# Optimization experiments

Hardware: AMD Instinct MI355X
Metric: run time of the kernel (lower is better)

The kernel has to match this reference:

```python
import jax, jax.numpy as jnp
import numpy as np

D_MODEL = 1024
NHEAD = 16
HEAD_DIM = D_MODEL // NHEAD


def setup_inputs() -> dict:
    key = jax.random.key(0)
    ks = jax.random.split(key, 6)
    scale = 0.02
    x = jax.random.normal(ks[0], (8, 1024, D_MODEL), dtype=jnp.float32)
    # nn.Linear weights are [out, in]; per-head q/k/v stacked over heads
    W_split = jax.random.normal(ks[1], (D_MODEL, D_MODEL), dtype=jnp.float32) * scale
    W_out = jax.random.normal(ks[2], (D_MODEL, D_MODEL), dtype=jnp.float32) * scale
    Wq = jax.random.normal(ks[3], (NHEAD, HEAD_DIM, HEAD_DIM), dtype=jnp.float32) * scale
    Wk = jax.random.normal(ks[4], (NHEAD, HEAD_DIM, HEAD_DIM), dtype=jnp.float32) * scale
    Wv = jax.random.normal(ks[5], (NHEAD, HEAD_DIM, HEAD_DIM), dtype=jnp.float32) * scale
    return {"x": x, "W_split": W_split, "W_out": W_out, "Wq": Wq, "Wk": Wk, "Wv": Wv}


def reference(x, W_split, W_out, Wq, Wk, Wv):
    b, s, _ = x.shape
    # x_proj: [b, s, h, hd]
    xp = (x @ W_split.T).reshape(b, s, NHEAD, HEAD_DIM)
    # per-head Linear (weight [out,in]): y = x @ W.T
    q = jnp.einsum('bshd,hod->bsho', xp, Wq)
    k = jnp.einsum('bshd,hod->bsho', xp, Wk)
    v = jnp.einsum('bshd,hod->bsho', xp, Wv)
    # scores scaled by sqrt(head_dim) (Attention.d_model == head_dim)
    scores = jnp.einsum('bsho,btho->bhst', q, k) / jnp.sqrt(jnp.float32(HEAD_DIM))
    attn = jax.nn.softmax(scores, axis=-1)  # [b, h, s, s]
    out = jnp.einsum('bhst,btho->bsho', attn, v)  # [b, s, h, hd]
    concat = out.reshape(b, s, D_MODEL)
    return concat @ W_out.T
```

## Files before the change

kernel.cpp:

```cpp
#include <hip/hip_runtime.h>
#include <math.h>

#define NHEAD 16
#define HD 64
#define DMODEL 1024
#define SEQ 1024
#define BATCH 8
#define ROWS (BATCH * SEQ)

typedef __attribute__((ext_vector_type(8))) short bf16x8;
typedef __attribute__((ext_vector_type(8))) short short8v;
typedef __attribute__((ext_vector_type(4))) float f32x4;
typedef __attribute__((ext_vector_type(16))) float f32x16;
typedef __attribute__((ext_vector_type(4))) short short4v;
typedef __attribute__((ext_vector_type(4))) unsigned int uint32x4;

__device__ __forceinline__ unsigned short f2bf(float f) {
    unsigned u = __builtin_bit_cast(unsigned, f);
    u += 0x7FFF + ((u >> 16) & 1);
    return (unsigned short)(u >> 16);
}

__device__ __forceinline__ float fexp2(float x) {
#if __has_builtin(__builtin_amdgcn_exp2f)
    return __builtin_amdgcn_exp2f(x);
#else
    return __expf(x * 0.6931471805599453f);
#endif
}

__device__ __forceinline__ void gload16(const void* g, void* l) {
    __builtin_amdgcn_global_load_lds(
        (const __attribute__((address_space(1))) unsigned int*)g,
        (__attribute__((address_space(3))) unsigned int*)l, 16, 0, 0);
}

__global__ __launch_bounds__(256) void cvt_bf16(const float* __restrict__ src,
                                                unsigned short* __restrict__ dst,
                                                int n, float scale) {
    int i = (blockIdx.x * 256 + threadIdx.x) * 8;
    if (i >= n) return;
    float4 a = *(const float4*)(src + i);
    float4 b = *(const float4*)(src + i + 4);
    short8v o;
    o[0] = (short)f2bf(a.x * scale); o[1] = (short)f2bf(a.y * scale);
    o[2] = (short)f2bf(a.z * scale); o[3] = (short)f2bf(a.w * scale);
    o[4] = (short)f2bf(b.x * scale); o[5] = (short)f2bf(b.y * scale);
    o[6] = (short)f2bf(b.z * scale); o[7] = (short)f2bf(b.w * scale);
    *(short8v*)(dst + i) = o;
}

__global__ __launch_bounds__(256) void gemm1_qkv(const unsigned short* __restrict__ A,
                                                 const unsigned short* __restrict__ B,
                                                 const unsigned short* __restrict__ wqb,
                                                 const unsigned short* __restrict__ wkb,
                                                 const unsigned short* __restrict__ wvb,
                                                 unsigned short* __restrict__ qb,
                                                 unsigned short* __restrict__ kbuf,
                                                 unsigned short* __restrict__ vT) {
    __shared__ char lds[65536];
    const int tid  = threadIdx.x;
    const int w    = tid >> 6;
    const int lane = tid & 63;
    const int lr   = lane & 15, lg = lane >> 4;
    const int wr   = w >> 1,  wc = w & 1;
    const int m0   = blockIdx.x * 128;
    const int n0   = blockIdx.y * 128;
    const int K    = DMODEL;

    f32x4 acc[4][4] = {};

    const int srow   = lane >> 3;
    const int swbyte = ((lane & 7) ^ srow) << 4;

#define G1_STAGE(buf, k0)                                                          \
    {                                                                              \
        _Pragma("unroll")                                                          \
        for (int c = 0; c < 4; ++c) {                                              \
            int chunk = w * 4 + c;                                                 \
            int row   = chunk * 8 + srow;                                          \
            gload16((const char*)A + ((size_t)(m0 + row) * K + (k0)) * 2 + swbyte, \
                    lds + (buf) * 16384 + chunk * 1024);                           \
            gload16((const char*)B + ((size_t)(n0 + row) * K + (k0)) * 2 + swbyte, \
                    lds + 32768 + (buf) * 16384 + chunk * 1024);                   \
        }                                                                          \
    }

    G1_STAGE(0, 0);
    __syncthreads();

    int cur = 0;
    for (int t = 0; t < K / 64; ++t) {
        if (t + 1 < K / 64) G1_STAGE(cur ^ 1, (t + 1) * 64);

#pragma unroll
        for (int k2 = 0; k2 < 2; ++k2) {
            bf16x8 af[4], bg[4];
#pragma unroll
            for (int f = 0; f < 4; ++f) {
                int row = wr * 64 + f * 16 + lr;
                af[f] = *(const bf16x8*)(lds + cur * 16384 + row * 128 +
                                         ((k2 * 64 + lg * 16) ^ ((row & 7) << 4)));
            }
#pragma unroll
            for (int g = 0; g < 4; ++g) {
                int row = wc * 64 + g * 16 + lr;
                bg[g] = *(const bf16x8*)(lds + 32768 + cur * 16384 + row * 128 +
                                         ((k2 * 64 + lg * 16) ^ ((row & 7) << 4)));
            }
#pragma unroll
            for (int f = 0; f < 4; ++f)
#pragma unroll
                for (int g = 0; g < 4; ++g)
                    acc[f][g] = __builtin_amdgcn_mfma_f32_16x16x32_bf16(af[f], bg[g],
                                                                        acc[f][g], 0, 0, 0);
        }
        __syncthreads();
        cur ^= 1;
    }
#undef G1_STAGE

#pragma unroll
    for (int f = 0; f < 4; ++f)
#pragma unroll
        for (int g = 0; g < 4; ++g)
#pragma unroll
            for (int r = 0; r < 4; ++r) {
                int mrow = wr * 64 + f * 16 + lg * 4 + r;
                int ncol = wc * 64 + g * 16 + lr;
                *(unsigned short*)(lds + mrow * 256 + ((ncol * 2) ^ ((mrow & 7) << 4))) =
                    f2bf(acc[f][g][r]);
            }

    const int b  = m0 >> 10;
    const int sl = m0 & 1023;

#pragma unroll
    for (int hh = 0; hh < 2; ++hh) {
        const int h = blockIdx.y * 2 + hh;
#pragma unroll
        for (int i = 0; i < 6; ++i) {
            int c   = w * 6 + i;
            int p   = c >> 3, rc = c & 7;
            int row = rc * 8 + srow;
            const unsigned short* ws = (p == 0) ? wqb : (p == 1) ? wkb : wvb;
            gload16((const char*)ws + ((size_t)(h * 64 + row) * 64) * 2 + swbyte,
                    lds + 32768 + p * 8192 + rc * 1024);
        }
        __syncthreads();

        f32x4 a2[3][2][4] = {};
#pragma unroll
        for (int k2 = 0; k2 < 2; ++k2) {
            bf16x8 af[2];
#pragma unroll
            for (int f = 0; f < 2; ++f) {
                int row = w * 32 + f * 16 + lr;
                af[f] = *(const bf16x8*)(lds + row * 256 +
                                         ((hh * 128 + k2 * 64 + lg * 16) ^ ((row & 7) << 4)));
            }
#pragma unroll
            for (int p = 0; p < 3; ++p)
#pragma unroll
                for (int g = 0; g < 4; ++g) {
                    int o = g * 16 + lr;
                    bf16x8 bg = *(const bf16x8*)(lds + 32768 + p * 8192 + o * 128 +
                                                 ((k2 * 64 + lg * 16) ^ ((o & 7) << 4)));
#pragma unroll
                    for (int f = 0; f < 2; ++f)
                        a2[p][f][g] = __builtin_amdgcn_mfma_f32_16x16x32_bf16(af[f], bg,
                                                                              a2[p][f][g], 0, 0, 0);
                }
        }

#pragma unroll
        for (int f = 0; f < 2; ++f)
#pragma unroll
            for (int g = 0; g < 4; ++g) {
#pragma unroll
                for (int r = 0; r < 4; ++r) {
                    size_t idx = (size_t)(m0 + w * 32 + f * 16 + lg * 4 + r) * DMODEL +
                                 h * 64 + g * 16 + lr;
                    qb[idx]   = f2bf(a2[0][f][g][r]);
                    kbuf[idx] = f2bf(a2[1][f][g][r]);
                }
                short4v pv;
#pragma unroll
                for (int r = 0; r < 4; ++r) pv[r] = (short)f2bf(a2[2][f][g][r]);
                size_t o = (size_t)(b * 16 + h) * 64 + g * 16 + lr;
                *(short4v*)(vT + o * SEQ + sl + w * 32 + f * 16 + lg * 4) = pv;
            }
        __syncthreads();
    }
}

__global__ __launch_bounds__(256) void gemm_bf16(const unsigned short* __restrict__ A,
                                                 const unsigned short* __restrict__ B,
                                                 float* __restrict__ Cf,
                                                 int M, int N, int K) {
    __shared__ char sA[2][16384];
    __shared__ char sB[2][16384];
    const int tid  = threadIdx.x;
    const int w    = tid >> 6;
    const int lane = tid & 63;
    const int lr   = lane & 15, lg = lane >> 4;
    const int wr   = w >> 1,  wc = w & 1;
    const int m0   = blockIdx.x * 128;
    const int n0   = blockIdx.y * 128;

    f32x4 acc[4][4] = {};

    const int srow   = lane >> 3;
    const int swbyte = ((lane & 7) ^ srow) << 4;
    const int nt     = K / 64;

#define GEMM_STAGE(buf, k0)                                                        \
    {                                                                              \
        _Pragma("unroll")                                                          \
        for (int c = 0; c < 4; ++c) {                                              \
            int chunk = w * 4 + c;                                                 \
            int row   = chunk * 8 + srow;                                          \
            gload16((const char*)A + ((size_t)(m0 + row) * K + (k0)) * 2 + swbyte, \
                    sA[buf] + chunk * 1024);                                       \
            gload16((const char*)B + ((size_t)(n0 + row) * K + (k0)) * 2 + swbyte, \
                    sB[buf] + chunk * 1024);                                       \
        }                                                                          \
    }

    GEMM_STAGE(0, 0);
    __syncthreads();

    int cur = 0;
    for (int t = 0; t < nt; ++t) {
        if (t + 1 < nt) GEMM_STAGE(cur ^ 1, (t + 1) * 64);

#pragma unroll
        for (int k2 = 0; k2 < 2; ++k2) {
            bf16x8 af[4], bg[4];
#pragma unroll
            for (int f = 0; f < 4; ++f) {
                int row = wr * 64 + f * 16 + lr;
                af[f] = *(const bf16x8*)(sA[cur] + row * 128 +
                                         ((k2 * 64 + lg * 16) ^ ((row & 7) << 4)));
            }
#pragma unroll
            for (int g = 0; g < 4; ++g) {
                int row = wc * 64 + g * 16 + lr;
                bg[g] = *(const bf16x8*)(sB[cur] + row * 128 +
                                         ((k2 * 64 + lg * 16) ^ ((row & 7) << 4)));
            }
#pragma unroll
            for (int f = 0; f < 4; ++f)
#pragma unroll
                for (int g = 0; g < 4; ++g)
                    acc[f][g] = __builtin_amdgcn_mfma_f32_16x16x32_bf16(af[f], bg[g],
                                                                        acc[f][g], 0, 0, 0);
        }
        __syncthreads();
        cur ^= 1;
    }
#undef GEMM_STAGE

#pragma unroll
    for (int f = 0; f < 4; ++f)
#pragma unroll
        for (int g = 0; g < 4; ++g)
#pragma unroll
            for (int r = 0; r < 4; ++r)
                Cf[(size_t)(m0 + wr * 64 + f * 16 + lg * 4 + r) * N +
                   n0 + wc * 64 + g * 16 + lr] = acc[f][g][r];
}

__global__ __launch_bounds__(512) void attn_mfma(const unsigned short* __restrict__ qb,
                                                 const unsigned short* __restrict__ kb,
                                                 const unsigned short* __restrict__ vT,
                                                 unsigned short* __restrict__ ob) {
    __shared__ unsigned short sK[4][4096];
    __shared__ unsigned short sV[4][4096];

    const int tid  = threadIdx.x;
    const int w    = tid >> 6;
    const int lane = tid & 63;
    const int ql   = lane & 31;
    const int hl   = lane >> 5;
    const int bh   = blockIdx.x;
    const int b    = bh >> 4, h = bh & 15;
    const int s0   = blockIdx.y * 256;
    const int NT   = SEQ / 64;

    const unsigned short* qrow = qb + ((size_t)(b * SEQ + s0 + w * 32 + ql) * DMODEL + h * 64);
    bf16x8 qf[4];
#pragma unroll
    for (int s = 0; s < 4; ++s)
        qf[s] = *(const bf16x8*)(qrow + 16 * s + 8 * hl);

    f32x16 acc0 = {}, acc1 = {};
    float m_ = -1e30f, l_ = 0.f;

    const int srow = lane >> 3;
    const int ssw  = ((lane & 7) << 4) ^ (srow << 4);
    const int swz  = (ql & 7) << 4;

#define ATTN_STAGE(buf, kt)                                                          \
    {                                                                                \
        int row = w * 8 + srow;                                                      \
        gload16((const char*)kb +                                                    \
                    (((size_t)(b * SEQ + (kt) * 64 + row) * DMODEL + h * 64) * 2) + ssw, \
                (char*)sK[buf] + w * 1024);                                          \
        gload16((const char*)vT +                                                    \
                    (((size_t)(bh * 64 + row) * SEQ + (kt) * 64) * 2) + ssw,         \
                (char*)sV[buf] + w * 1024);                                          \
    }

    ATTN_STAGE(0, 0);
    ATTN_STAGE(1, 1);
    asm volatile("s_waitcnt vmcnt(2)" ::: "memory");
    __builtin_amdgcn_s_barrier();
    __builtin_amdgcn_sched_barrier(0);

    for (int kt = 0; kt < NT; ++kt) {
        const int cb = kt & 3;
        if (kt + 2 < NT) ATTN_STAGE((kt + 2) & 3, kt + 2);

        f32x16 st0 = {}, st1 = {};
        __builtin_amdgcn_s_setprio(1);
#pragma unroll
        for (int s = 0; s < 4; ++s) {
            int byo = (32 * s + 16 * hl) ^ swz;
            bf16x8 kf0 = *(const bf16x8*)((const char*)sK[cb] + ql * 128 + byo);
            bf16x8 kf1 = *(const bf16x8*)((const char*)sK[cb] + (32 + ql) * 128 + byo);
            st0 = __builtin_amdgcn_mfma_f32_32x32x16_bf16(kf0, qf[s], st0, 0, 0, 0);
            st1 = __builtin_amdgcn_mfma_f32_32x32x16_bf16(kf1, qf[s], st1, 0, 0, 0);
        }
        __builtin_amdgcn_s_setprio(0);

        float mx = st0[0];
#pragma unroll
        for (int i = 1; i < 16; ++i) mx = fmaxf(mx, st0[i]);
#pragma unroll
        for (int i = 0; i < 16; ++i) mx = fmaxf(mx, st1[i]);
        if (__any(mx > m_ + 8.f)) {
            float rm = fmaxf(mx, __shfl_xor(mx, 32, 64));
            float mn = fmaxf(m_, rm);
            float al = fexp2(m_ - mn);
            m_ = mn;
            l_ *= al;
#pragma unroll
            for (int i = 0; i < 16; ++i) { acc0[i] *= al; acc1[i] *= al; }
        }

        bf16x8 pf[4];
        float lsum = 0.f;
#define TILE_P(stv, PF0, PF1)                                                       \
        {                                                                           \
            float p_[16];                                                           \
            _Pragma("unroll")                                                       \
            for (int i = 0; i < 16; ++i) {                                          \
                p_[i] = fexp2(stv[i] - m_);                                         \
                lsum += p_[i];                                                      \
            }                                                                       \
            unsigned pk_[8];                                                        \
            _Pragma("unroll")                                                       \
            for (int i = 0; i < 8; ++i)                                             \
                asm("v_cvt_pk_bf16_f32 %0, %1, %2"                                  \
                    : "=v"(pk_[i]) : "v"(p_[2 * i]), "v"(p_[2 * i + 1]));           \
            auto rA = __builtin_amdgcn_permlane32_swap(pk_[0], pk_[2], false, false); \
            auto rB = __builtin_amdgcn_permlane32_swap(pk_[1], pk_[3], false, false); \
            auto rC = __builtin_amdgcn_permlane32_swap(pk_[4], pk_[6], false, false); \
            auto rD = __builtin_amdgcn_permlane32_swap(pk_[5], pk_[7], false, false); \
            uint32x4 f0, f1;                                                        \
            f0[0] = rA[0]; f0[1] = rB[0]; f0[2] = rA[1]; f0[3] = rB[1];             \
            f1[0] = rC[0]; f1[1] = rD[0]; f1[2] = rC[1]; f1[3] = rD[1];             \
            PF0 = __builtin_bit_cast(bf16x8, f0);                                   \
            PF1 = __builtin_bit_cast(bf16x8, f1);                                   \
        }
        TILE_P(st0, pf[0], pf[1]);
        TILE_P(st1, pf[2], pf[3]);
#undef TILE_P
        l_ += lsum;

        __builtin_amdgcn_s_setprio(1);
#pragma unroll
        for (int s = 0; s < 4; ++s) {
            int byo = (32 * s + 16 * hl) ^ swz;
            bf16x8 vf0 = *(const bf16x8*)((const char*)sV[cb] + ql * 128 + byo);
            bf16x8 vf1 = *(const bf16x8*)((const char*)sV[cb] + (32 + ql) * 128 + byo);
            acc0 = __builtin_amdgcn_mfma_f32_32x32x16_bf16(vf0, pf[s], acc0, 0, 0, 0);
            acc1 = __builtin_amdgcn_mfma_f32_32x32x16_bf16(vf1, pf[s], acc1, 0, 0, 0);
        }
        __builtin_amdgcn_s_setprio(0);

        if (kt + 2 < NT) { asm volatile("s_waitcnt vmcnt(2)" ::: "memory"); }
        else             { asm volatile("s_waitcnt vmcnt(0)" ::: "memory"); }
        __builtin_amdgcn_s_barrier();
        __builtin_amdgcn_sched_barrier(0);
    }
#undef ATTN_STAGE

    float lf  = l_ + __shfl_xor(l_, 32, 64);
    float inv = 1.f / lf;
    const size_t rowbase = (size_t)(b * SEQ + s0 + w * 32 + ql) * DMODEL + h * 64;
#pragma unroll
    for (int reg = 0; reg < 16; ++reg) {
        int d = (reg & 3) + 8 * (reg >> 2) + 4 * hl;
        ob[rowbase + d]      = f2bf(acc0[reg] * inv);
        ob[rowbase + 32 + d] = f2bf(acc1[reg] * inv);
    }
}

#define QSCALE 0.18033688011112042f
extern "C" void kernel_launch(void* const* d_in, const int* in_sizes, int n_in,
                              void* d_out, int out_size, void* d_ws, size_t ws_size,
                              hipStream_t stream) {
    const float* x       = (const float*)d_in[0];
    const float* W_split = (const float*)d_in[1];
    const float* W_out   = (const float*)d_in[2];
    const float* Wq      = (const float*)d_in[3];
    const float* Wk      = (const float*)d_in[4];
    const float* Wv      = (const float*)d_in[5];
    float* out = (float*)d_out;

    unsigned short* xb  = (unsigned short*)d_ws;
    unsigned short* obb = xb;
    unsigned short* wsb = xb + (size_t)ROWS * DMODEL;
    unsigned short* wob = wsb + (size_t)DMODEL * DMODEL;
    unsigned short* qbuf= wob + (size_t)DMODEL * DMODEL;
    unsigned short* kbuf= qbuf + (size_t)ROWS * DMODEL;
    unsigned short* vT  = kbuf + (size_t)ROWS * DMODEL;
    unsigned short* wqb = vT + (size_t)ROWS * DMODEL;
    unsigned short* wkb = wqb + (size_t)NHEAD * HD * HD;
    unsigned short* wvb = wkb + (size_t)NHEAD * HD * HD;

    dim3 blk(256);

    cvt_bf16<<<dim3(ROWS * DMODEL / 2048), blk, 0, stream>>>(x, xb, ROWS * DMODEL, 1.f);
    cvt_bf16<<<dim3(DMODEL * DMODEL / 2048), blk, 0, stream>>>(W_split, wsb, DMODEL * DMODEL, 1.f);
    cvt_bf16<<<dim3(DMODEL * DMODEL / 2048), blk, 0, stream>>>(W_out, wob, DMODEL * DMODEL, 1.f);
    cvt_bf16<<<dim3(NHEAD * HD * HD / 2048), blk, 0, stream>>>(Wq, wqb, NHEAD * HD * HD, QSCALE);
    cvt_bf16<<<dim3(NHEAD * HD * HD / 2048), blk, 0, stream>>>(Wk, wkb, NHEAD * HD * HD, 1.f);
    cvt_bf16<<<dim3(NHEAD * HD * HD / 2048), blk, 0, stream>>>(Wv, wvb, NHEAD * HD * HD, 1.f);

    gemm1_qkv<<<dim3(ROWS / 128, DMODEL / 128), blk, 0, stream>>>(
        xb, wsb, wqb, wkb, wvb, qbuf, kbuf, vT);
    attn_mfma<<<dim3(BATCH * NHEAD, SEQ / 256), dim3(512), 0, stream>>>(qbuf, kbuf, vT, obb);
    gemm_bf16<<<dim3(ROWS / 128, DMODEL / 128), blk, 0, stream>>>(
        obb, wob, out, ROWS, DMODEL, DMODEL);
}
```

Measured before the change: 128.6 us.

## Fuse conversion launches, compute softmax denominator via MFMA, vectorize output stores

Merges the six bf16 conversion kernels into one launch, which removes per-launch overhead for the small weight tensors. In the attention loop, the row sum of probabilities is now computed by an extra MFMA against a ones vector instead of scalar adds, and the row max uses a tree reduction. Output stores are packed into 4-wide short vectors. The extra MFMA adds matrix work and accumulator registers per tile in exchange for fewer VALU adds; the ones-MFMA sum uses bf16-rounded probabilities, which slightly changes numerics.

```diff
diff --git a/kernel.cpp b/kernel.cpp
--- a/kernel.cpp
+++ b/kernel.cpp
@@ -35,11 +35,28 @@
         (__attribute__((address_space(3))) unsigned int*)l, 16, 0, 0);
 }
 
-__global__ __launch_bounds__(256) void cvt_bf16(const float* __restrict__ src,
-                                                unsigned short* __restrict__ dst,
-                                                int n, float scale) {
-    int i = (blockIdx.x * 256 + threadIdx.x) * 8;
-    if (i >= n) return;
+#define QSCALE 0.18033688011112042f
+__global__ __launch_bounds__(256) void cvt_all(const float* __restrict__ x,
+                                               const float* __restrict__ Ws,
+                                               const float* __restrict__ Wo,
+                                               const float* __restrict__ Wq,
+                                               const float* __restrict__ Wk,
+                                               const float* __restrict__ Wv,
+                                               unsigned short* __restrict__ xb,
+                                               unsigned short* __restrict__ wsb,
+                                               unsigned short* __restrict__ wob,
+                                               unsigned short* __restrict__ wqb,
+                                               unsigned short* __restrict__ wkb,
+                                               unsigned short* __restrict__ wvb) {
+    int bid = blockIdx.x;
+    const float* src; unsigned short* dst; float scale = 1.f;
+    if (bid < 4096)      { src = x;  dst = xb;  }
+    else if (bid < 4608) { src = Ws; dst = wsb; bid -= 4096; }
+    else if (bid < 5120) { src = Wo; dst = wob; bid -= 4608; }
+    else if (bid < 5152) { src = Wq; dst = wqb; bid -= 5120; scale = QSCALE; }
+    else if (bid < 5184) { src = Wk; dst = wkb; bid -= 5152; }
+    else                 { src = Wv; dst = wvb; bid -= 5184; }
+    int i = (bid * 256 + threadIdx.x) * 8;
     float4 a = *(const float4*)(src + i);
     float4 b = *(const float4*)(src + i + 4);
     short8v o;
@@ -294,8 +311,12 @@
     for (int s = 0; s < 4; ++s)
         qf[s] = *(const bf16x8*)(qrow + 16 * s + 8 * hl);
 
-    f32x16 acc0 = {}, acc1 = {};
-    float m_ = -1e30f, l_ = 0.f;
+    bf16x8 ones;
+#pragma unroll
+    for (int e = 0; e < 8; ++e) ones[e] = (short)0x3F80;
+
+    f32x16 acc0 = {}, acc1 = {}, accl = {};
+    float m_ = -1e30f;
 
     const int srow = lane >> 3;
     const int ssw  = ((lane & 7) << 4) ^ (srow << 4);
@@ -334,31 +355,33 @@
         }
         __builtin_amdgcn_s_setprio(0);
 
-        float mx = st0[0];
-#pragma unroll
-        for (int i = 1; i < 16; ++i) mx = fmaxf(mx, st0[i]);
-#pragma unroll
-        for (int i = 0; i < 16; ++i) mx = fmaxf(mx, st1[i]);
+        float a4[8];
+#pragma unroll
+        for (int i = 0; i < 4; ++i)
+            a4[i] = fmaxf(fmaxf(st0[4 * i], st0[4 * i + 1]),
+                          fmaxf(st0[4 * i + 2], st0[4 * i + 3]));
+#pragma unroll
+        for (int i = 0; i < 4; ++i)
+            a4[4 + i] = fmaxf(fmaxf(st1[4 * i], st1[4 * i + 1]),
+                              fmaxf(st1[4 * i + 2], st1[4 * i + 3]));
+        float mx = fmaxf(fmaxf(fmaxf(a4[0], a4[1]), fmaxf(a4[2], a4[3])),
+                         fmaxf(fmaxf(a4[4], a4[5]), fmaxf(a4[6], a4[7])));
         if (__any(mx > m_ + 8.f)) {
             float rm = fmaxf(mx, __shfl_xor(mx, 32, 64));
             float mn = fmaxf(m_, rm);
             float al = fexp2(m_ - mn);
             m_ = mn;
-            l_ *= al;
+            accl[0] *= al;
 #pragma unroll
             for (int i = 0; i < 16; ++i) { acc0[i] *= al; acc1[i] *= al; }
         }
 
         bf16x8 pf[4];
-        float lsum = 0.f;
 #define TILE_P(stv, PF0, PF1)                                                       \
         {                                                                           \
             float p_[16];                                                           \
             _Pragma("unroll")                                                       \
-            for (int i = 0; i < 16; ++i) {                                          \
-                p_[i] = fexp2(stv[i] - m_);                                         \
-                lsum += p_[i];                                                      \
-            }                                                                       \
+            for (int i = 0; i < 16; ++i) p_[i] = fexp2(stv[i] - m_);                \
             unsigned pk_[8];                                                        \
             _Pragma("unroll")                                                       \
             for (int i = 0; i < 8; ++i)                                             \
@@ -377,7 +400,6 @@
         TILE_P(st0, pf[0], pf[1]);
         TILE_P(st1, pf[2], pf[3]);
 #undef TILE_P
-        l_ += lsum;
 
         __builtin_amdgcn_s_setprio(1);
 #pragma unroll
@@ -387,6 +409,7 @@
             bf16x8 vf1 = *(const bf16x8*)((const char*)sV[cb] + (32 + ql) * 128 + byo);
             acc0 = __builtin_amdgcn_mfma_f32_32x32x16_bf16(vf0, pf[s], acc0, 0, 0, 0);
             acc1 = __builtin_amdgcn_mfma_f32_32x32x16_bf16(vf1, pf[s], acc1, 0, 0, 0);
+            accl = __builtin_amdgcn_mfma_f32_32x32x16_bf16(ones, pf[s], accl, 0, 0, 0);
         }
         __builtin_amdgcn_s_setprio(0);
 
@@ -397,18 +420,22 @@
     }
 #undef ATTN_STAGE
 
-    float lf  = l_ + __shfl_xor(l_, 32, 64);
-    float inv = 1.f / lf;
+    float inv = 1.f / accl[0];
     const size_t rowbase = (size_t)(b * SEQ + s0 + w * 32 + ql) * DMODEL + h * 64;
 #pragma unroll
-    for (int reg = 0; reg < 16; ++reg) {
-        int d = (reg & 3) + 8 * (reg >> 2) + 4 * hl;
-        ob[rowbase + d]      = f2bf(acc0[reg] * inv);
-        ob[rowbase + 32 + d] = f2bf(acc1[reg] * inv);
-    }
-}
-
-#define QSCALE 0.18033688011112042f
+    for (int g = 0; g < 4; ++g) {
+        short4v o0, o1;
+#pragma unroll
+        for (int r = 0; r < 4; ++r) {
+            o0[r] = (short)f2bf(acc0[4 * g + r] * inv);
+            o1[r] = (short)f2bf(acc1[4 * g + r] * inv);
+        }
+        int d = 8 * g + 4 * hl;
+        *(short4v*)(ob + rowbase + d)      = o0;
+        *(short4v*)(ob + rowbase + 32 + d) = o1;
+    }
+}
+
 extern "C" void kernel_launch(void* const* d_in, const int* in_sizes, int n_in,
                               void* d_out, int out_size, void* d_ws, size_t ws_size,
                               hipStream_t stream) {
@@ -433,13 +460,8 @@
 
     dim3 blk(256);
 
-    cvt_bf16<<<dim3(ROWS * DMODEL / 2048), blk, 0, stream>>>(x, xb, ROWS * DMODEL, 1.f);
-    cvt_bf16<<<dim3(DMODEL * DMODEL / 2048), blk, 0, stream>>>(W_split, wsb, DMODEL * DMODEL, 1.f);
-    cvt_bf16<<<dim3(DMODEL * DMODEL / 2048), blk, 0, stream>>>(W_out, wob, DMODEL * DMODEL, 1.f);
-    cvt_bf16<<<dim3(NHEAD * HD * HD / 2048), blk, 0, stream>>>(Wq, wqb, NHEAD * HD * HD, QSCALE);
-    cvt_bf16<<<dim3(NHEAD * HD * HD / 2048), blk, 0, stream>>>(Wk, wkb, NHEAD * HD * HD, 1.f);
-    cvt_bf16<<<dim3(NHEAD * HD * HD / 2048), blk, 0, stream>>>(Wv, wvb, NHEAD * HD * HD, 1.f);
-
+    cvt_all<<<dim3(5216), blk, 0, stream>>>(x, W_split, W_out, Wq, Wk, Wv,
+                                            xb, wsb, wob, wqb, wkb, wvb);
     gemm1_qkv<<<dim3(ROWS / 128, DMODEL / 128), blk, 0, stream>>>(
         xb, wsb, wqb, wkb, wvb, qbuf, kbuf, vT);
     attn_mfma<<<dim3(BATCH * NHEAD, SEQ / 256), dim3(512), 0, stream>>>(qbuf, kbuf, vT, obb);
```

Measured after the change: 131.1 us. No clear change (+1.9%).
